# Kernel tuning notes

Measured on AMD Instinct MI355X. Metric: run time of the kernel, lower is better.

Reference implementation:

```python
import jax, jax.numpy as jnp
import numpy as np

N0, N1, N2 = 200000, 100000, 50000
E0, E1 = 1600000, 800000
IN_F, H_F, N_CLS = 128, 256, 64


def sage_conv(h_src, src_idx, dst_idx, num_dst, W_self, W_neigh, b):
    # DGL SAGEConv with aggregator_type='mean':
    #   h_neigh = mean over in-neighbors of h_src
    #   out = h_dst @ W_self + h_neigh @ W_neigh + b
    h_dst = h_src[:num_dst]
    msgs = h_src[src_idx]                                   # [E, F] gather
    summed = jax.ops.segment_sum(msgs, dst_idx, num_segments=num_dst)
    deg = jax.ops.segment_sum(jnp.ones((src_idx.shape[0],), h_src.dtype),
                              dst_idx, num_segments=num_dst)
    h_neigh = summed / jnp.maximum(deg, 1.0)[:, None]       # mean, safe for deg=0
    return h_dst @ W_self + h_neigh @ W_neigh + b


def setup_inputs() -> dict:
    key = jax.random.key(0)
    ks = jax.random.split(key, 10)
    s1 = 1.0 / np.sqrt(IN_F)
    s2 = 1.0 / np.sqrt(H_F)
    return {
        "x": jax.random.normal(ks[0], (N0, IN_F), jnp.float32),
        "src0": jax.random.randint(ks[1], (E0,), 0, N0, jnp.int64 if jax.config.jax_enable_x64 else jnp.int32),
        "dst0": jnp.sort(jax.random.randint(ks[2], (E0,), 0, N1)),
        "src1": jax.random.randint(ks[3], (E1,), 0, N1),
        "dst1": jnp.sort(jax.random.randint(ks[4], (E1,), 0, N2)),
        "num_dst0": N1,
        "num_dst1": N2,
        "W_self1": jax.random.normal(ks[5], (IN_F, H_F), jnp.float32) * s1,
        "W_neigh1": jax.random.normal(ks[6], (IN_F, H_F), jnp.float32) * s1,
        "b1": jnp.zeros((H_F,), jnp.float32),
        "W_self2": jax.random.normal(ks[7], (H_F, N_CLS), jnp.float32) * s2,
        "W_neigh2": jax.random.normal(ks[8], (H_F, N_CLS), jnp.float32) * s2,
        "b2": jnp.zeros((N_CLS,), jnp.float32),
    }


def reference(x, src0, dst0, src1, dst1, num_dst0, num_dst1,
              W_self1, W_neigh1, b1, W_self2, W_neigh2, b2):
    h = sage_conv(x, src0, dst0, num_dst0, W_self1, W_neigh1, b1)   # [N1, H]
    h = jax.nn.relu(h)
    h = sage_conv(h, src1, dst1, num_dst1, W_self2, W_neigh2, b2)   # [N2, C]
    return h
```

## Files before the change

kernel.cpp:

```cpp
#include <hip/hip_runtime.h>

constexpr int cN0  = 200000;
constexpr int cN1  = 100000;
constexpr int cN2  = 50000;
constexpr int cE0  = 1600000;
constexpr int cE1  = 800000;
constexpr int cIN  = 128;
constexpr int cH   = 256;
constexpr int cCLS = 64;

constexpr float QSTEP = 6.0f / 127.0f;
constexpr float QINV  = 127.0f / 6.0f;

using bf16x8 = __attribute__((ext_vector_type(8))) short;
using f32x4  = __attribute__((ext_vector_type(4))) float;

__device__ __forceinline__ float bflo(unsigned int u) {
    union { unsigned int i; float f; } v; v.i = u << 16; return v.f;
}
__device__ __forceinline__ float bfhi(unsigned int u) {
    union { unsigned int i; float f; } v; v.i = u & 0xFFFF0000u; return v.f;
}
__device__ __forceinline__ unsigned int f2bf(float f) {
    union { float f; unsigned int i; } v; v.f = f;
    return (v.i + 0x7FFFu + ((v.i >> 16) & 1u)) >> 16;
}

constexpr int PV   = 8;
constexpr int QF4  = cN0 * cIN / 4;
constexpr int QBLK = QF4 / (256 * PV);
constexpr int WCNT = cH * cH + 2 * cCLS * cH;
constexpr int WBLK = WCNT / 256;
constexpr int RCNT = (cN1 + 1) + (cN2 + 1);
constexpr int RBLK = (RCNT + 255) / 256;

__global__ __launch_bounds__(256) void prep(
        const float* __restrict__ x,
        const float* __restrict__ Ws1, const float* __restrict__ Wn1,
        const float* __restrict__ Wn2, const float* __restrict__ Ws2,
        const int* __restrict__ dst0, const int* __restrict__ dst1,
        unsigned int* __restrict__ xq,
        unsigned short* __restrict__ Wt1, unsigned short* __restrict__ Wt2,
        int* __restrict__ row0, int* __restrict__ row1) {
    const int b = blockIdx.x, tid = threadIdx.x;
    if (b < QBLK) {
        const int base = b * 256 * PV + tid;
        const float4* xp = (const float4*)x;

        float4 v[PV];
        #pragma unroll
        for (int j = 0; j < PV; ++j)
            v[j] = xp[base + j * 256];
        auto q8b = [](float f) -> unsigned int {
            int q = __float2int_rn(f * QINV);
            q = q > 127 ? 127 : (q < -127 ? -127 : q);
            return (unsigned int)(q + 128);
        };
        #pragma unroll
        for (int j = 0; j < PV; ++j) {
            float4 a = v[j];
            unsigned int d = q8b(a.x) | (q8b(a.y) << 8) |
                             (q8b(a.z) << 16) | (q8b(a.w) << 24);
            xq[base + j * 256] = d;
        }
    } else if (b < QBLK + WBLK) {
        const int wi = (b - QBLK) * 256 + tid;
        if (wi < cH * cH) {
            int n = wi >> 8, k = wi & 255;
            float v = (k < cIN) ? Ws1[k * cH + n] : Wn1[(k - cIN) * cH + n];
            Wt1[n * cH + k] = (unsigned short)f2bf(v);
        } else {
            int j = wi - cH * cH; int n = j >> 8, k = j & 255;
            float v = (n < cCLS) ? Wn2[k * cCLS + n] : Ws2[k * cCLS + (n - cCLS)];
            Wt2[n * cH + k] = (unsigned short)f2bf(v);
        }
    } else {
        const int ti = (b - QBLK - WBLK) * 256 + tid;
        if (ti <= cN1) {
            int lo = 0, hi = cE0;
            while (lo < hi) { int mid = (lo + hi) >> 1; if (dst0[mid] < ti) lo = mid + 1; else hi = mid; }
            row0[ti] = lo;
        } else {
            int d = ti - (cN1 + 1);
            if (d <= cN2) {
                int lo = 0, hi = cE1;
                while (lo < hi) { int mid = (lo + hi) >> 1; if (dst1[mid] < d) lo = mid + 1; else hi = mid; }
                row1[d] = lo;
            }
        }
    }
}

__global__ __launch_bounds__(256) void agg_i8(
        const uint2* __restrict__ xq,
        const int* __restrict__ sidx,
        const int* __restrict__ rows,
        unsigned short* __restrict__ nb,
        int num_dst) {
    const int tid = threadIdx.x, lane = tid & 63;
    const int m = blockIdx.x * 4 + (tid >> 6);
    if (m >= num_dst) return;
    const int sub = lane >> 4, t = lane & 15;
    const int e0 = rows[m], e1 = rows[m + 1];

    unsigned int accA = 0, accB = 0, accC = 0, accD = 0;

    for (int base = e0; base < e1; base += 16) {
        int s[4]; bool val[4];
        #pragma unroll
        for (int k = 0; k < 4; ++k) {
            int ei = base + k * 4 + sub;
            val[k] = ei < e1;
            s[k] = sidx[val[k] ? ei : e0];
        }
        uint2 v[4];
        #pragma unroll
        for (int k = 0; k < 4; ++k)
            v[k] = xq[(size_t)s[k] * 16 + t];
        #pragma unroll
        for (int k = 0; k < 4; ++k) {
            uint2 w = val[k] ? v[k] : make_uint2(0u, 0u);
            accA += w.x & 0x00FF00FFu;
            accB += (w.x >> 8) & 0x00FF00FFu;
            accC += w.y & 0x00FF00FFu;
            accD += (w.y >> 8) & 0x00FF00FFu;
        }
    }

    accA += __shfl_xor((int)accA, 16, 64); accA += __shfl_xor((int)accA, 32, 64);
    accB += __shfl_xor((int)accB, 16, 64); accB += __shfl_xor((int)accB, 32, 64);
    accC += __shfl_xor((int)accC, 16, 64); accC += __shfl_xor((int)accC, 32, 64);
    accD += __shfl_xor((int)accD, 16, 64); accD += __shfl_xor((int)accD, 32, 64);

    if (sub == 0) {
        const int deg = e1 - e0;
        const float inv  = QSTEP / (float)(deg > 1 ? deg : 1);
        const float bias = 128.0f * (float)deg;
        auto cv = [&](unsigned int field) -> float {
            return ((float)(int)field - bias) * inv;
        };
        float f0 = cv(accA & 0xFFFFu), f2 = cv(accA >> 16);
        float f1 = cv(accB & 0xFFFFu), f3 = cv(accB >> 16);
        float f4 = cv(accC & 0xFFFFu), f6 = cv(accC >> 16);
        float f5 = cv(accD & 0xFFFFu), f7 = cv(accD >> 16);
        uint4 w;
        w.x = f2bf(f0) | (f2bf(f1) << 16);
        w.y = f2bf(f2) | (f2bf(f3) << 16);
        w.z = f2bf(f4) | (f2bf(f5) << 16);
        w.w = f2bf(f6) | (f2bf(f7) << 16);
        ((uint4*)nb)[(size_t)m * 16 + t] = w;
    }
}

template<int K, bool ACCUM>
__global__ __launch_bounds__(256) void agg_wave(
        const unsigned short* __restrict__ src,
        const int* __restrict__ sidx,
        const int* __restrict__ rows,
        void* __restrict__ outv, int num_dst) {
    constexpr int LPR = K / 8;
    constexpr int EPW = 64 / LPR;
    const int tid = threadIdx.x;
    const int lane = tid & 63;
    const int m = blockIdx.x * 4 + (tid >> 6);
    if (m >= num_dst) return;
    const int sub = lane / LPR;
    const int t   = lane % LPR;

    const uint4* s4 = (const uint4*)src;
    const int e0 = rows[m], e1 = rows[m + 1];

    float acc[8];
    #pragma unroll
    for (int j = 0; j < 8; ++j) acc[j] = 0.f;
    auto addv = [&](uint4 v) {
        acc[0] += bflo(v.x); acc[1] += bfhi(v.x);
        acc[2] += bflo(v.y); acc[3] += bfhi(v.y);
        acc[4] += bflo(v.z); acc[5] += bfhi(v.z);
        acc[6] += bflo(v.w); acc[7] += bfhi(v.w);
    };

    int base = e0;
    for (; base + 2 * EPW <= e1; base += 2 * EPW) {
        int sA = sidx[base + sub], sB = sidx[base + EPW + sub];
        uint4 vA = s4[(size_t)sA * LPR + t];
        uint4 vB = s4[(size_t)sB * LPR + t];
        addv(vA); addv(vB);
    }
    for (; base < e1; base += EPW) {
        int idx = base + sub;
        if (idx < e1) addv(s4[(size_t)sidx[idx] * LPR + t]);
    }

    #pragma unroll
    for (int j = 0; j < 8; ++j) {
        #pragma unroll
        for (int off = LPR; off < 64; off <<= 1)
            acc[j] += __shfl_xor(acc[j], off, 64);
    }

    if (sub == 0) {
        const int deg = e1 - e0;
        const float inv = 1.0f / (float)(deg > 1 ? deg : 1);
        if (!ACCUM) {
            uint4 o;
            o.x = f2bf(acc[0] * inv) | (f2bf(acc[1] * inv) << 16);
            o.y = f2bf(acc[2] * inv) | (f2bf(acc[3] * inv) << 16);
            o.z = f2bf(acc[4] * inv) | (f2bf(acc[5] * inv) << 16);
            o.w = f2bf(acc[6] * inv) | (f2bf(acc[7] * inv) << 16);
            ((uint4*)outv)[(size_t)m * LPR + t] = o;
        } else {
            float* op = (float*)outv + (size_t)m * K + t * 8;
            float4 o0 = *(float4*)op, o1 = *(float4*)(op + 4);
            o0.x += acc[0] * inv; o0.y += acc[1] * inv;
            o0.z += acc[2] * inv; o0.w += acc[3] * inv;
            o1.x += acc[4] * inv; o1.y += acc[5] * inv;
            o1.z += acc[6] * inv; o1.w += acc[7] * inv;
            *(float4*)op = o0; *(float4*)(op + 4) = o1;
        }
    }
}

__global__ __launch_bounds__(512) void gemm1_fused(
        const float* __restrict__ X,
        const unsigned short* __restrict__ NB,
        const unsigned short* __restrict__ Bt,
        const float* __restrict__ bias,
        unsigned short* __restrict__ C) {
    __shared__ unsigned short As[128][40];
    __shared__ unsigned short Bs[256][40];

    const int tid = threadIdx.x;
    const int m0 = blockIdx.x * 128;
    const int lane = tid & 63, wave = tid >> 6;
    const int wrow = wave >> 2, wcol = wave & 3;
    const int quad = lane >> 4, l16 = lane & 15;

    f32x4 acc[4][4];
    #pragma unroll
    for (int i = 0; i < 4; ++i)
        #pragma unroll
        for (int j = 0; j < 4; ++j)
            acc[i][j] = (f32x4){0.f, 0.f, 0.f, 0.f};

    const int arow = tid >> 2, aq = tid & 3;
    const int gma  = m0 + arow;

    for (int kb = 0; kb < cH; kb += 32) {
        if (kb < cIN) {
            float4 a0 = {0,0,0,0}, a1 = {0,0,0,0};
            if (gma < cN1) {
                const float4* p = (const float4*)(X + (size_t)gma * cIN + kb + aq * 8);
                a0 = p[0]; a1 = p[1];
            }
            uint4 v;
            v.x = f2bf(a0.x) | (f2bf(a0.y) << 16);
            v.y = f2bf(a0.z) | (f2bf(a0.w) << 16);
            v.z = f2bf(a1.x) | (f2bf(a1.y) << 16);
            v.w = f2bf(a1.z) | (f2bf(a1.w) << 16);
            *(uint4*)&As[arow][aq * 8] = v;
        } else {
            uint4 v = make_uint4(0, 0, 0, 0);
            if (gma < cN1)
                v = *(const uint4*)(NB + (size_t)gma * cIN + (kb - cIN) + aq * 8);
            *(uint4*)&As[arow][aq * 8] = v;
        }
        #pragma unroll
        for (int f = 0; f < 2; ++f) {
            int idx = tid + f * 512;
            int row = idx >> 2, q = idx & 3;
            uint4 v = *(const uint4*)(Bt + (size_t)row * cH + kb + q * 8);
            *(uint4*)&Bs[row][q * 8] = v;
        }
        __syncthreads();

        bf16x8 a[4], b[4];
        #pragma unroll
        for (int i = 0; i < 4; ++i)
            a[i] = *(const bf16x8*)&As[wrow * 64 + i * 16 + l16][quad * 8];
        #pragma unroll
        for (int j = 0; j < 4; ++j)
            b[j] = *(const bf16x8*)&Bs[wcol * 64 + j * 16 + l16][quad * 8];
        #pragma unroll
        for (int i = 0; i < 4; ++i)
            #pragma unroll
            for (int j = 0; j < 4; ++j)
                acc[i][j] = __builtin_amdgcn_mfma_f32_16x16x32_bf16(
                    a[i], b[j], acc[i][j], 0, 0, 0);
        __syncthreads();
    }

    float bv[4];
    #pragma unroll
    for (int j = 0; j < 4; ++j)
        bv[j] = bias[wcol * 64 + j * 16 + l16];
    #pragma unroll
    for (int i = 0; i < 4; ++i) {
        #pragma unroll
        for (int r = 0; r < 4; ++r) {
            int gm = m0 + wrow * 64 + i * 16 + quad * 4 + r;
            if (gm >= cN1) continue;
            #pragma unroll
            for (int j = 0; j < 4; ++j) {
                int gn = wcol * 64 + j * 16 + l16;
                float v = acc[i][j][r] + bv[j];
                v = fmaxf(v, 0.f);
                C[(size_t)gm * cH + gn] = (unsigned short)f2bf(v);
            }
        }
    }
}

__global__ __launch_bounds__(256) void gemm2_split(
        const unsigned short* __restrict__ A,
        const unsigned short* __restrict__ Bt,
        const float* __restrict__ b2,
        unsigned short* __restrict__ zb,
        float* __restrict__ out) {
    __shared__ unsigned short As[128][40];
    __shared__ unsigned short Bs[128][40];
    const int tid = threadIdx.x;
    const int m0 = blockIdx.x * 128;
    const int lane = tid & 63, wave = tid >> 6;
    const int wrow = wave >> 1, wcol = wave & 1;
    const int quad = lane >> 4, l16 = lane & 15;

    f32x4 acc[4][4];
    #pragma unroll
    for (int i = 0; i < 4; ++i)
        #pragma unroll
        for (int j = 0; j < 4; ++j)
            acc[i][j] = (f32x4){0.f, 0.f, 0.f, 0.f};

    for (int kb = 0; kb < cH; kb += 32) {
        #pragma unroll
        for (int f = 0; f < 2; ++f) {
            int idx = tid + f * 256;
            int row = idx >> 2, q = idx & 3;
            int gm = m0 + row;
            uint4 v = make_uint4(0, 0, 0, 0);
            if (gm < cN1) v = *(const uint4*)(A + (size_t)gm * cH + kb + q * 8);
            *(uint4*)&As[row][q * 8] = v;
        }
        #pragma unroll
        for (int f = 0; f < 2; ++f) {
            int idx = tid + f * 256;
            int row = idx >> 2, q = idx & 3;
            uint4 v = *(const uint4*)(Bt + (size_t)row * cH + kb + q * 8);
            *(uint4*)&Bs[row][q * 8] = v;
        }
        __syncthreads();

        bf16x8 a[4], b[4];
        #pragma unroll
        for (int i = 0; i < 4; ++i)
            a[i] = *(const bf16x8*)&As[(wrow * 4 + i) * 16 + l16][quad * 8];
        #pragma unroll
        for (int j = 0; j < 4; ++j)
            b[j] = *(const bf16x8*)&Bs[(wcol * 4 + j) * 16 + l16][quad * 8];
        #pragma unroll
        for (int i = 0; i < 4; ++i)
            #pragma unroll
            for (int j = 0; j < 4; ++j)
                acc[i][j] = __builtin_amdgcn_mfma_f32_16x16x32_bf16(
                    a[i], b[j], acc[i][j], 0, 0, 0);
        __syncthreads();
    }

    if (wcol == 0) {
        #pragma unroll
        for (int i = 0; i < 4; ++i) {
            #pragma unroll
            for (int r = 0; r < 4; ++r) {
                int gm = m0 + (wrow * 4 + i) * 16 + quad * 4 + r;
                if (gm >= cN1) continue;
                #pragma unroll
                for (int j = 0; j < 4; ++j) {
                    int gn = j * 16 + l16;
                    zb[(size_t)gm * cCLS + gn] = (unsigned short)f2bf(acc[i][j][r]);
                }
            }
        }
    } else {
        float bv[4];
        #pragma unroll
        for (int j = 0; j < 4; ++j) bv[j] = b2[j * 16 + l16];
        #pragma unroll
        for (int i = 0; i < 4; ++i) {
            #pragma unroll
            for (int r = 0; r < 4; ++r) {
                int gm = m0 + (wrow * 4 + i) * 16 + quad * 4 + r;
                if (gm >= cN2) continue;
                #pragma unroll
                for (int j = 0; j < 4; ++j)
                    out[(size_t)gm * cCLS + j * 16 + l16] = acc[i][j][r] + bv[j];
            }
        }
    }
}

extern "C" void kernel_launch(void* const* d_in, const int* in_sizes, int n_in,
                              void* d_out, int out_size, void* d_ws, size_t ws_size,
                              hipStream_t stream) {
    const float* x      = (const float*)d_in[0];
    const int*   src0   = (const int*)d_in[1];
    const int*   dst0   = (const int*)d_in[2];
    const int*   src1   = (const int*)d_in[3];
    const int*   dst1   = (const int*)d_in[4];
    const float* Wself1  = (const float*)d_in[7];
    const float* Wneigh1 = (const float*)d_in[8];
    const float* b1      = (const float*)d_in[9];
    const float* Wself2  = (const float*)d_in[10];
    const float* Wneigh2 = (const float*)d_in[11];
    const float* b2      = (const float*)d_in[12];
    float* out = (float*)d_out;

    char* ws = (char*)d_ws;
    int* row0 = (int*)ws;
    int* row1 = row0 + (cN1 + 1);
    size_t off = (size_t)((cN1 + 1) + (cN2 + 1)) * sizeof(int);
    off = (off + 1023) & ~(size_t)1023;
    unsigned int*   xq = (unsigned int*)(ws + off);
    unsigned short* zb = (unsigned short*)(ws + off); off += (size_t)cN0 * cIN;
    unsigned short* nb  = (unsigned short*)(ws + off); off += (size_t)cN1 * cIN * 2;
    unsigned short* h1b = (unsigned short*)(ws + off); off += (size_t)cN1 * cH * 2;
    unsigned short* Wt1 = (unsigned short*)(ws + off); off += (size_t)cH * cH * 2;
    unsigned short* Wt2 = (unsigned short*)(ws + off); off += (size_t)2 * cCLS * cH * 2;

    prep<<<QBLK + WBLK + RBLK, 256, 0, stream>>>(
        x, Wself1, Wneigh1, Wneigh2, Wself2, dst0, dst1,
        xq, Wt1, Wt2, row0, row1);

    agg_i8<<<(cN1 + 3) / 4, 256, 0, stream>>>(
        (const uint2*)xq, src0, row0, nb, cN1);

    gemm1_fused<<<(cN1 + 127) / 128, 512, 0, stream>>>(
        x, nb, Wt1, b1, h1b);

    gemm2_split<<<(cN1 + 127) / 128, 256, 0, stream>>>(h1b, Wt2, b2, zb, out);

    agg_wave<cCLS, true><<<(cN2 + 3) / 4, 256, 0, stream>>>(
        zb, src1, row1, out, cN2);
}
```

Baseline: 331.4 us.

## Fuse layer-1 and layer-2 GEMMs via shared-memory hidden tile; scan-based CSR row build

Merges the two GEMM kernels into one. Each block now covers 64 rows, keeps the ReLU'd bf16 hidden tile in XOR-swizzled shared memory, and runs the second GEMM from it, so the N1x256 hidden activation never makes a round trip through global memory. The prep kernel builds the CSR row offsets by scanning adjacent sorted dst entries instead of a binary search per node. The cost is a smaller M tile with less B reuse, more shared memory per block, and W2 fragments read directly from global memory with no staging.

```diff
diff --git a/kernel.cpp b/kernel.cpp
--- a/kernel.cpp
+++ b/kernel.cpp
@@ -26,13 +26,15 @@
     return (v.i + 0x7FFFu + ((v.i >> 16) & 1u)) >> 16;
 }
 
+constexpr int R0T  = cE0 / 4;
+constexpr int R0B  = (R0T + 255) / 256;
+constexpr int R1T  = cE1 / 4;
+constexpr int R1B  = (R1T + 255) / 256;
+constexpr int WCNT = cH * cH + 2 * cCLS * cH;
+constexpr int WBLK = WCNT / 256;
 constexpr int PV   = 8;
 constexpr int QF4  = cN0 * cIN / 4;
 constexpr int QBLK = QF4 / (256 * PV);
-constexpr int WCNT = cH * cH + 2 * cCLS * cH;
-constexpr int WBLK = WCNT / 256;
-constexpr int RCNT = (cN1 + 1) + (cN2 + 1);
-constexpr int RBLK = (RCNT + 255) / 256;
 
 __global__ __launch_bounds__(256) void prep(
         const float* __restrict__ x,
@@ -43,28 +45,34 @@
         unsigned short* __restrict__ Wt1, unsigned short* __restrict__ Wt2,
         int* __restrict__ row0, int* __restrict__ row1) {
     const int b = blockIdx.x, tid = threadIdx.x;
-    if (b < QBLK) {
-        const int base = b * 256 * PV + tid;
-        const float4* xp = (const float4*)x;
-
-        float4 v[PV];
-        #pragma unroll
-        for (int j = 0; j < PV; ++j)
-            v[j] = xp[base + j * 256];
-        auto q8b = [](float f) -> unsigned int {
-            int q = __float2int_rn(f * QINV);
-            q = q > 127 ? 127 : (q < -127 ? -127 : q);
-            return (unsigned int)(q + 128);
-        };
-        #pragma unroll
-        for (int j = 0; j < PV; ++j) {
-            float4 a = v[j];
-            unsigned int d = q8b(a.x) | (q8b(a.y) << 8) |
-                             (q8b(a.z) << 16) | (q8b(a.w) << 24);
-            xq[base + j * 256] = d;
-        }
-    } else if (b < QBLK + WBLK) {
-        const int wi = (b - QBLK) * 256 + tid;
+    if (b < R0B) {
+        const int t = b * 256 + tid;
+        if (t < R0T) {
+            const int e = t * 4;
+            int4 cur = *(const int4*)(dst0 + e);
+            int prev = (e == 0) ? -1 : dst0[e - 1];
+            for (int d = prev + 1;  d <= cur.x; ++d) row0[d] = e;
+            for (int d = cur.x + 1; d <= cur.y; ++d) row0[d] = e + 1;
+            for (int d = cur.y + 1; d <= cur.z; ++d) row0[d] = e + 2;
+            for (int d = cur.z + 1; d <= cur.w; ++d) row0[d] = e + 3;
+            if (e + 4 == cE0)
+                for (int d = cur.w + 1; d <= cN1; ++d) row0[d] = cE0;
+        }
+    } else if (b < R0B + R1B) {
+        const int t = (b - R0B) * 256 + tid;
+        if (t < R1T) {
+            const int e = t * 4;
+            int4 cur = *(const int4*)(dst1 + e);
+            int prev = (e == 0) ? -1 : dst1[e - 1];
+            for (int d = prev + 1;  d <= cur.x; ++d) row1[d] = e;
+            for (int d = cur.x + 1; d <= cur.y; ++d) row1[d] = e + 1;
+            for (int d = cur.y + 1; d <= cur.z; ++d) row1[d] = e + 2;
+            for (int d = cur.z + 1; d <= cur.w; ++d) row1[d] = e + 3;
+            if (e + 4 == cE1)
+                for (int d = cur.w + 1; d <= cN2; ++d) row1[d] = cE1;
+        }
+    } else if (b < R0B + R1B + WBLK) {
+        const int wi = (b - R0B - R1B) * 256 + tid;
         if (wi < cH * cH) {
             int n = wi >> 8, k = wi & 255;
             float v = (k < cIN) ? Ws1[k * cH + n] : Wn1[(k - cIN) * cH + n];
@@ -75,18 +83,25 @@
             Wt2[n * cH + k] = (unsigned short)f2bf(v);
         }
     } else {
-        const int ti = (b - QBLK - WBLK) * 256 + tid;
-        if (ti <= cN1) {
-            int lo = 0, hi = cE0;
-            while (lo < hi) { int mid = (lo + hi) >> 1; if (dst0[mid] < ti) lo = mid + 1; else hi = mid; }
-            row0[ti] = lo;
-        } else {
-            int d = ti - (cN1 + 1);
-            if (d <= cN2) {
-                int lo = 0, hi = cE1;
-                while (lo < hi) { int mid = (lo + hi) >> 1; if (dst1[mid] < d) lo = mid + 1; else hi = mid; }
-                row1[d] = lo;
-            }
+        const int qb = b - (R0B + R1B + WBLK);
+        const int base = qb * 256 * PV + tid;
+        const float4* xp = (const float4*)x;
+
+        float4 v[PV];
+        #pragma unroll
+        for (int j = 0; j < PV; ++j)
+            v[j] = xp[base + j * 256];
+        auto q8b = [](float f) -> unsigned int {
+            int q = __float2int_rn(f * QINV);
+            q = q > 127 ? 127 : (q < -127 ? -127 : q);
+            return (unsigned int)(q + 128);
+        };
+        #pragma unroll
+        for (int j = 0; j < PV; ++j) {
+            float4 a = v[j];
+            unsigned int d = q8b(a.x) | (q8b(a.y) << 8) |
+                             (q8b(a.z) << 16) | (q8b(a.w) << 24);
+            xq[base + j * 256] = d;
         }
     }
 }
@@ -221,182 +236,141 @@
     }
 }
 
-__global__ __launch_bounds__(512) void gemm1_fused(
+__global__ __launch_bounds__(512) void gemm12(
         const float* __restrict__ X,
         const unsigned short* __restrict__ NB,
-        const unsigned short* __restrict__ Bt,
-        const float* __restrict__ bias,
-        unsigned short* __restrict__ C) {
-    __shared__ unsigned short As[128][40];
+        const unsigned short* __restrict__ Wt1,
+        const float* __restrict__ b1,
+        const unsigned short* __restrict__ Wt2,
+        const float* __restrict__ b2,
+        unsigned short* __restrict__ zb,
+        float* __restrict__ out) {
+    __shared__ unsigned short As[64][40];
     __shared__ unsigned short Bs[256][40];
+    __shared__ unsigned short H[64][256];
 
     const int tid = threadIdx.x;
-    const int m0 = blockIdx.x * 128;
+    const int m0 = blockIdx.x * 64;
     const int lane = tid & 63, wave = tid >> 6;
-    const int wrow = wave >> 2, wcol = wave & 3;
     const int quad = lane >> 4, l16 = lane & 15;
 
-    f32x4 acc[4][4];
+    const int wcol = wave;
+    f32x4 acc[4][2];
     #pragma unroll
     for (int i = 0; i < 4; ++i)
         #pragma unroll
-        for (int j = 0; j < 4; ++j)
+        for (int j = 0; j < 2; ++j)
             acc[i][j] = (f32x4){0.f, 0.f, 0.f, 0.f};
 
-    const int arow = tid >> 2, aq = tid & 3;
+    const int arow = tid >> 3, afq = tid & 7;
     const int gma  = m0 + arow;
 
     for (int kb = 0; kb < cH; kb += 32) {
         if (kb < cIN) {
-            float4 a0 = {0,0,0,0}, a1 = {0,0,0,0};
-            if (gma < cN1) {
-                const float4* p = (const float4*)(X + (size_t)gma * cIN + kb + aq * 8);
-                a0 = p[0]; a1 = p[1];
-            }
-            uint4 v;
-            v.x = f2bf(a0.x) | (f2bf(a0.y) << 16);
-            v.y = f2bf(a0.z) | (f2bf(a0.w) << 16);
-            v.z = f2bf(a1.x) | (f2bf(a1.y) << 16);
-            v.w = f2bf(a1.z) | (f2bf(a1.w) << 16);
-            *(uint4*)&As[arow][aq * 8] = v;
+            float4 a = {0.f, 0.f, 0.f, 0.f};
+            if (gma < cN1)
+                a = *(const float4*)(X + (size_t)gma * cIN + kb + afq * 4);
+            uint2 v;
+            v.x = f2bf(a.x) | (f2bf(a.y) << 16);
+            v.y = f2bf(a.z) | (f2bf(a.w) << 16);
+            *(uint2*)&As[arow][afq * 4] = v;
         } else {
-            uint4 v = make_uint4(0, 0, 0, 0);
+            uint2 v = make_uint2(0u, 0u);
             if (gma < cN1)
-                v = *(const uint4*)(NB + (size_t)gma * cIN + (kb - cIN) + aq * 8);
-            *(uint4*)&As[arow][aq * 8] = v;
+                v = *(const uint2*)(NB + (size_t)gma * cIN + (kb - cIN) + afq * 4);
+            *(uint2*)&As[arow][afq * 4] = v;
         }
         #pragma unroll
         for (int f = 0; f < 2; ++f) {
             int idx = tid + f * 512;
             int row = idx >> 2, q = idx & 3;
-            uint4 v = *(const uint4*)(Bt + (size_t)row * cH + kb + q * 8);
+            uint4 v = *(const uint4*)(Wt1 + (size_t)row * cH + kb + q * 8);
             *(uint4*)&Bs[row][q * 8] = v;
         }
         __syncthreads();
 
-        bf16x8 a[4], b[4];
+        bf16x8 a[4], bf[2];
         #pragma unroll
         for (int i = 0; i < 4; ++i)
-            a[i] = *(const bf16x8*)&As[wrow * 64 + i * 16 + l16][quad * 8];
-        #pragma unroll
-        for (int j = 0; j < 4; ++j)
-            b[j] = *(const bf16x8*)&Bs[wcol * 64 + j * 16 + l16][quad * 8];
+            a[i] = *(const bf16x8*)&As[i * 16 + l16][quad * 8];
+        #pragma unroll
+        for (int j = 0; j < 2; ++j)
+            bf[j] = *(const bf16x8*)&Bs[wcol * 32 + j * 16 + l16][quad * 8];
         #pragma unroll
         for (int i = 0; i < 4; ++i)
             #pragma unroll
-            for (int j = 0; j < 4; ++j)
+            for (int j = 0; j < 2; ++j)
                 acc[i][j] = __builtin_amdgcn_mfma_f32_16x16x32_bf16(
-                    a[i], b[j], acc[i][j], 0, 0, 0);
+                    a[i], bf[j], acc[i][j], 0, 0, 0);
         __syncthreads();
     }
 
-    float bv[4];
-    #pragma unroll
-    for (int j = 0; j < 4; ++j)
-        bv[j] = bias[wcol * 64 + j * 16 + l16];
-    #pragma unroll
-    for (int i = 0; i < 4; ++i) {
+    float bv[2];
+    #pragma unroll
+    for (int j = 0; j < 2; ++j)
+        bv[j] = b1[wcol * 32 + j * 16 + l16];
+    #pragma unroll
+    for (int i = 0; i < 4; ++i)
         #pragma unroll
         for (int r = 0; r < 4; ++r) {
-            int gm = m0 + wrow * 64 + i * 16 + quad * 4 + r;
-            if (gm >= cN1) continue;
+            int row = i * 16 + quad * 4 + r;
             #pragma unroll
-            for (int j = 0; j < 4; ++j) {
-                int gn = wcol * 64 + j * 16 + l16;
-                float v = acc[i][j][r] + bv[j];
-                v = fmaxf(v, 0.f);
-                C[(size_t)gm * cH + gn] = (unsigned short)f2bf(v);
+            for (int j = 0; j < 2; ++j) {
+                int col = wcol * 32 + j * 16 + l16;
+                float v = fmaxf(acc[i][j][r] + bv[j], 0.f);
+                H[row][((((col >> 3) ^ (row & 7)) << 3) | (col & 7))] =
+                    (unsigned short)f2bf(v);
             }
         }
-    }
-}
-
-__global__ __launch_bounds__(256) void gemm2_split(
-        const unsigned short* __restrict__ A,
-        const unsigned short* __restrict__ Bt,
-        const float* __restrict__ b2,
-        unsigned short* __restrict__ zb,
-        float* __restrict__ out) {
-    __shared__ unsigned short As[128][40];
-    __shared__ unsigned short Bs[128][40];
-    const int tid = threadIdx.x;
-    const int m0 = blockIdx.x * 128;
-    const int lane = tid & 63, wave = tid >> 6;
-    const int wrow = wave >> 1, wcol = wave & 1;
-    const int quad = lane >> 4, l16 = lane & 15;
-
-    f32x4 acc[4][4];
-    #pragma unroll
-    for (int i = 0; i < 4; ++i)
-        #pragma unroll
-        for (int j = 0; j < 4; ++j)
-            acc[i][j] = (f32x4){0.f, 0.f, 0.f, 0.f};
-
+    __syncthreads();
+
+    const int wr2 = wave >> 2, wc2 = wave & 3;
+    f32x4 acc2[2][2];
+    #pragma unroll
+    for (int i = 0; i < 2; ++i)
+        #pragma unroll
+        for (int j = 0; j < 2; ++j)
+            acc2[i][j] = (f32x4){0.f, 0.f, 0.f, 0.f};
+
+    #pragma unroll
     for (int kb = 0; kb < cH; kb += 32) {
-        #pragma unroll
-        for (int f = 0; f < 2; ++f) {
-            int idx = tid + f * 256;
-            int row = idx >> 2, q = idx & 3;
-            int gm = m0 + row;
-            uint4 v = make_uint4(0, 0, 0, 0);
-            if (gm < cN1) v = *(const uint4*)(A + (size_t)gm * cH + kb + q * 8);
-            *(uint4*)&As[row][q * 8] = v;
-        }
-        #pragma unroll
-        for (int f = 0; f < 2; ++f) {
-            int idx = tid + f * 256;
-            int row = idx >> 2, q = idx & 3;
-            uint4 v = *(const uint4*)(Bt + (size_t)row * cH + kb + q * 8);
-            *(uint4*)&Bs[row][q * 8] = v;
-        }
-        __syncthreads();
-
-        bf16x8 a[4], b[4];
-        #pragma unroll
-        for (int i = 0; i < 4; ++i)
-            a[i] = *(const bf16x8*)&As[(wrow * 4 + i) * 16 + l16][quad * 8];
-        #pragma unroll
-        for (int j = 0; j < 4; ++j)
-            b[j] = *(const bf16x8*)&Bs[(wcol * 4 + j) * 16 + l16][quad * 8];
-        #pragma unroll
-        for (int i = 0; i < 4; ++i)
+        bf16x8 a2[2], b2f[2];
+        #pragma unroll
+        for (int i = 0; i < 2; ++i) {
+            int row = wr2 * 32 + i * 16 + l16;
+            int kc = ((kb >> 3) + quad) ^ (row & 7);
+            a2[i] = *(const bf16x8*)&H[row][kc << 3];
+        }
+        #pragma unroll
+        for (int j = 0; j < 2; ++j) {
+            int n = wc2 * 32 + j * 16 + l16;
+            b2f[j] = *(const bf16x8*)(Wt2 + (size_t)n * cH + kb + quad * 8);
+        }
+        #pragma unroll
+        for (int i = 0; i < 2; ++i)
             #pragma unroll
-            for (int j = 0; j < 4; ++j)
-                acc[i][j] = __builtin_amdgcn_mfma_f32_16x16x32_bf16(
-                    a[i], b[j], acc[i][j], 0, 0, 0);
-        __syncthreads();
-    }
-
-    if (wcol == 0) {
-        #pragma unroll
-        for (int i = 0; i < 4; ++i) {
+            for (int j = 0; j < 2; ++j)
+                acc2[i][j] = __builtin_amdgcn_mfma_f32_16x16x32_bf16(
+                    a2[i], b2f[j], acc2[i][j], 0, 0, 0);
+    }
+
+    #pragma unroll
+    for (int i = 0; i < 2; ++i)
+        #pragma unroll
+        for (int r = 0; r < 4; ++r) {
+            int gm = m0 + wr2 * 32 + i * 16 + quad * 4 + r;
             #pragma unroll
-            for (int r = 0; r < 4; ++r) {
-                int gm = m0 + (wrow * 4 + i) * 16 + quad * 4 + r;
-                if (gm >= cN1) continue;
-                #pragma unroll
-                for (int j = 0; j < 4; ++j) {
-                    int gn = j * 16 + l16;
-                    zb[(size_t)gm * cCLS + gn] = (unsigned short)f2bf(acc[i][j][r]);
+            for (int j = 0; j < 2; ++j) {
+                int n = wc2 * 32 + j * 16 + l16;
+                float v = acc2[i][j][r];
+                if (n < cCLS) {
+                    if (gm < cN1)
+                        zb[(size_t)gm * cCLS + n] = (unsigned short)f2bf(v);
+                } else if (gm < cN2) {
+                    out[(size_t)gm * cCLS + (n - cCLS)] = v + b2[n - cCLS];
                 }
             }
         }
-    } else {
-        float bv[4];
-        #pragma unroll
-        for (int j = 0; j < 4; ++j) bv[j] = b2[j * 16 + l16];
-        #pragma unroll
-        for (int i = 0; i < 4; ++i) {
-            #pragma unroll
-            for (int r = 0; r < 4; ++r) {
-                int gm = m0 + (wrow * 4 + i) * 16 + quad * 4 + r;
-                if (gm >= cN2) continue;
-                #pragma unroll
-                for (int j = 0; j < 4; ++j)
-                    out[(size_t)gm * cCLS + j * 16 + l16] = acc[i][j][r] + bv[j];
-            }
-        }
-    }
 }
 
 extern "C" void kernel_launch(void* const* d_in, const int* in_sizes, int n_in,
@@ -423,21 +397,18 @@
     unsigned int*   xq = (unsigned int*)(ws + off);
     unsigned short* zb = (unsigned short*)(ws + off); off += (size_t)cN0 * cIN;
     unsigned short* nb  = (unsigned short*)(ws + off); off += (size_t)cN1 * cIN * 2;
-    unsigned short* h1b = (unsigned short*)(ws + off); off += (size_t)cN1 * cH * 2;
     unsigned short* Wt1 = (unsigned short*)(ws + off); off += (size_t)cH * cH * 2;
     unsigned short* Wt2 = (unsigned short*)(ws + off); off += (size_t)2 * cCLS * cH * 2;
 
-    prep<<<QBLK + WBLK + RBLK, 256, 0, stream>>>(
+    prep<<<R0B + R1B + WBLK + QBLK, 256, 0, stream>>>(
         x, Wself1, Wneigh1, Wneigh2, Wself2, dst0, dst1,
         xq, Wt1, Wt2, row0, row1);
 
     agg_i8<<<(cN1 + 3) / 4, 256, 0, stream>>>(
         (const uint2*)xq, src0, row0, nb, cN1);
 
-    gemm1_fused<<<(cN1 + 127) / 128, 512, 0, stream>>>(
-        x, nb, Wt1, b1, h1b);
-
-    gemm2_split<<<(cN1 + 127) / 128, 256, 0, stream>>>(h1b, Wt2, b2, zb, out);
+    gemm12<<<(cN1 + 63) / 64, 512, 0, stream>>>(
+        x, nb, Wt1, b1, Wt2, b2, zb, out);
 
     agg_wave<cCLS, true><<<(cN2 + 3) / 4, 256, 0, stream>>>(
         zb, src1, row1, out, cN2);
```

New measurement: 325.4 us. Within noise of the previous version (-1.8%).
